# Kernel optimization log

Hardware: AMD Instinct MI355X
Metric: run time of the kernel (lower is better)

Reference implementation:

```python
import jax, jax.numpy as jnp
import numpy as np


def setup_inputs() -> dict:
    key = jax.random.key(0)
    ks = jax.random.split(key, 7)
    B, Hde, E, Hf, Wf, Catt = 256, 512, 512, 8, 32, 512
    return {
        "h": jax.random.normal(ks[0], (B, Hde), dtype=jnp.float32),
        "x_em": jax.random.normal(ks[1], (B, E, Hf, Wf), dtype=jnp.float32),
        "att_x_em": jax.random.normal(ks[2], (B, Hf * Wf, Catt), dtype=jnp.float32),
        "Wh": jax.random.normal(ks[3], (E, Hde), dtype=jnp.float32) * (1.0 / np.sqrt(Hde)),
        "bh": jax.random.normal(ks[4], (E,), dtype=jnp.float32) * 0.02,
        "Wa": jax.random.normal(ks[5], (E,), dtype=jnp.float32) * (1.0 / np.sqrt(E)),
        "ba": jax.random.normal(ks[6], (), dtype=jnp.float32) * 0.02,
        "feature_h": Hf,
        "feature_w": Wf,
    }


def reference(h, x_em, att_x_em, Wh, bh, Wa, ba, feature_h, feature_w):
    # h: [B, Hde]; 1x1 conv on [B,Hde,1,1] == linear layer
    B = h.shape[0]
    g_em = h @ Wh.T + bh                                   # [B, E]
    # broadcast-add g_em over spatial, tanh (dropout = identity in eval)
    feat = jnp.tanh(x_em + g_em[:, :, None, None])         # [B, E, H, W]
    # conv_att: 1x1 conv E -> 1 == weighted channel sum
    scores = jnp.einsum('behw,e->bhw', feat, Wa) + ba      # [B, H, W]
    alpha = jax.nn.softmax(scores.reshape(B, feature_h * feature_w), axis=-1)  # [B, HW]
    att_out = jnp.einsum('bs,bsc->bc', alpha, att_x_em)    # [B, Catt]
    return att_out, alpha.reshape(B, 1, feature_h * feature_w)
```

## Files before the change

kernel.cpp:

```cpp
#include <hip/hip_runtime.h>

#define BB 256
#define E 512
#define HDE 512
#define HW 256
#define CATT 512
#define EC 8
#define ECH (E / EC)
#define SC 8
#define SCH (HW / SC)


__device__ __forceinline__ float fast_tanh(float x) {
    float t = __expf(2.0f * x);
    return 1.0f - 2.0f / (t + 1.0f);
}

__global__ __launch_bounds__(256, 4) void kA(
        const float* __restrict__ h, const float* __restrict__ x_em,
        const float* __restrict__ Wh, const float* __restrict__ bh,
        const float* __restrict__ Wa, float* __restrict__ scoresPart) {
    const int b = blockIdx.x;
    const int ec = blockIdx.y;
    const int t = threadIdx.x;

    __shared__ float sH[HDE];
    __shared__ float sG[ECH];
    __shared__ float sWa[ECH];
    __shared__ float4 sPart[4][HW / 4];

    if (t < HDE / 4) {
        ((float4*)sH)[t] = ((const float4*)(h + (size_t)b * HDE))[t];
    }
    __syncthreads();

    {
        const int el = t >> 2;
        const int ks = t & 3;
        const int e = ec * ECH + el;
        const float* wrow = Wh + (size_t)e * HDE;
        float acc = 0.0f;
#pragma unroll
        for (int i = 0; i < HDE / 16; ++i) {
            const int k = ks * 4 + i * 16;
            float4 w = *(const float4*)(wrow + k);
            float4 hv = *(const float4*)(sH + k);
            acc += w.x * hv.x + w.y * hv.y + w.z * hv.z + w.w * hv.w;
        }
        acc += __shfl_xor(acc, 1);
        acc += __shfl_xor(acc, 2);
        if (ks == 0) {
            sG[el] = acc + bh[e];
            sWa[el] = Wa[e];
        }
    }
    __syncthreads();

    const int s4 = t & 63;
    const int esub = t >> 6;
    const float* xb = x_em + ((size_t)b * E + (size_t)ec * ECH) * HW + s4 * 4;
    float4 acc = {0.f, 0.f, 0.f, 0.f};
#pragma unroll 4
    for (int i = 0; i < ECH / 4; ++i) {
        const int el = 4 * i + esub;
        float4 x = *(const float4*)(xb + (size_t)el * HW);
        const float g = sG[el];
        const float wa = sWa[el];
        acc.x += wa * fast_tanh(x.x + g);
        acc.y += wa * fast_tanh(x.y + g);
        acc.z += wa * fast_tanh(x.z + g);
        acc.w += wa * fast_tanh(x.w + g);
    }

    sPart[esub][s4] = acc;
    __syncthreads();
    if (t < HW / 4) {
        float4 r0 = sPart[0][t], r1 = sPart[1][t], r2 = sPart[2][t], r3 = sPart[3][t];
        float4 r;
        r.x = r0.x + r1.x + r2.x + r3.x;
        r.y = r0.y + r1.y + r2.y + r3.y;
        r.z = r0.z + r1.z + r2.z + r3.z;
        r.w = r0.w + r1.w + r2.w + r3.w;
        *(float4*)(scoresPart + ((size_t)ec * BB + b) * HW + t * 4) = r;
    }
}

__global__ __launch_bounds__(256, 4) void kB(
        const float* __restrict__ scoresPart, float* __restrict__ out) {
    const int b = blockIdx.x;
    const int t = threadIdx.x;
    float v = 0.0f;
#pragma unroll
    for (int ec = 0; ec < EC; ++ec)
        v += scoresPart[((size_t)ec * BB + b) * HW + t];

    __shared__ float sred[4];
    const int wid = t >> 6;

    float m = v;
#pragma unroll
    for (int o = 32; o; o >>= 1) m = fmaxf(m, __shfl_xor(m, o));
    if ((t & 63) == 0) sred[wid] = m;
    __syncthreads();
    m = fmaxf(fmaxf(sred[0], sred[1]), fmaxf(sred[2], sred[3]));
    __syncthreads();

    float p = __expf(v - m);
    float s = p;
#pragma unroll
    for (int o = 32; o; o >>= 1) s += __shfl_xor(s, o);
    if ((t & 63) == 0) sred[wid] = s;
    __syncthreads();
    s = sred[0] + sred[1] + sred[2] + sred[3];

    out[(size_t)BB * CATT + (size_t)b * HW + t] = p / s;
}

__global__ __launch_bounds__(256, 8) void kC(
        const float* __restrict__ att, const float* __restrict__ alpha,
        float* __restrict__ outPart) {
    const int b = blockIdx.x;
    const int sc = blockIdx.y;
    const int t = threadIdx.x;
    const int c4 = t & 127;
    const int sp = t >> 7;

    __shared__ float sA[SCH];
    __shared__ float4 sP[CATT / 4];

    if (t < SCH) sA[t] = alpha[(size_t)b * HW + sc * SCH + t];
    __syncthreads();

    const float* ab = att + ((size_t)b * HW + (size_t)sc * SCH) * CATT + c4 * 4;
    float4 acc = {0.f, 0.f, 0.f, 0.f};
#pragma unroll 4
    for (int i = 0; i < SCH / 2; ++i) {
        const int s = 2 * i + sp;
        float4 x = *(const float4*)(ab + (size_t)s * CATT);
        const float a = sA[s];
        acc.x += a * x.x;
        acc.y += a * x.y;
        acc.z += a * x.z;
        acc.w += a * x.w;
    }
    if (sp == 1) sP[c4] = acc;
    __syncthreads();
    if (sp == 0) {
        float4 o = sP[c4];
        acc.x += o.x; acc.y += o.y; acc.z += o.z; acc.w += o.w;
        *(float4*)(outPart + ((size_t)sc * BB + b) * CATT + c4 * 4) = acc;
    }
}

__global__ __launch_bounds__(128, 8) void kD(
        const float* __restrict__ outPart, float* __restrict__ out) {
    const int b = blockIdx.x;
    const int t = threadIdx.x;
    float4 acc = {0.f, 0.f, 0.f, 0.f};
#pragma unroll
    for (int sc = 0; sc < SC; ++sc) {
        float4 x = *(const float4*)(outPart + ((size_t)sc * BB + b) * CATT + t * 4);
        acc.x += x.x; acc.y += x.y; acc.z += x.z; acc.w += x.w;
    }
    *(float4*)(out + (size_t)b * CATT + t * 4) = acc;
}

extern "C" void kernel_launch(void* const* d_in, const int* in_sizes, int n_in,
                              void* d_out, int out_size, void* d_ws, size_t ws_size,
                              hipStream_t stream) {
    const float* h      = (const float*)d_in[0];
    const float* x_em   = (const float*)d_in[1];
    const float* att    = (const float*)d_in[2];
    const float* Wh     = (const float*)d_in[3];
    const float* bh     = (const float*)d_in[4];
    const float* Wa     = (const float*)d_in[5];

    float* out = (float*)d_out;
    float* scoresPart = (float*)d_ws;
    float* outPart = (float*)d_ws + (size_t)EC * BB * HW;

    kA<<<dim3(BB, EC), 256, 0, stream>>>(h, x_em, Wh, bh, Wa, scoresPart);
    kB<<<dim3(BB), 256, 0, stream>>>(scoresPart, out);
    kC<<<dim3(BB, SC), 256, 0, stream>>>(att, out + (size_t)BB * CATT, outPart);
    kD<<<dim3(BB), 128, 0, stream>>>(outPart, out);
}
```

Measured before the change: 307.2 us.

## Fuse four attention kernels into one per-batch 1024-thread block

Replaces the four-kernel pipeline (score partials, softmax, weighted-sum partials, final reduction) with a single kernel. Each 1024-thread block handles one batch row end to end and keeps scores, alpha and partial sums in shared memory. This removes workspace round trips and three launch boundaries, and tanh now uses a hardware reciprocal. The cost is a grid of only 256 large blocks, with fewer waves in flight to hide memory latency and more per-block serialization between phases.

```diff
diff --git a/kernel.cpp b/kernel.cpp
--- a/kernel.cpp
+++ b/kernel.cpp
@@ -5,182 +5,142 @@
 #define HDE 512
 #define HW 256
 #define CATT 512
-#define EC 8
-#define ECH (E / EC)
-#define SC 8
-#define SCH (HW / SC)
-
+#define NT 1024
+#define NW (NT / 64)
 
 __device__ __forceinline__ float fast_tanh(float x) {
-    float t = __expf(2.0f * x);
-    return 1.0f - 2.0f / (t + 1.0f);
+    float e = __expf(2.0f * x);
+    float r = __builtin_amdgcn_rcpf(1.0f + e);
+    return 1.0f - 2.0f * r;
 }
 
-__global__ __launch_bounds__(256, 4) void kA(
+__global__ __launch_bounds__(NT, 4) void fused_attn(
         const float* __restrict__ h, const float* __restrict__ x_em,
-        const float* __restrict__ Wh, const float* __restrict__ bh,
-        const float* __restrict__ Wa, float* __restrict__ scoresPart) {
+        const float* __restrict__ att, const float* __restrict__ Wh,
+        const float* __restrict__ bh, const float* __restrict__ Wa,
+        float* __restrict__ out) {
     const int b = blockIdx.x;
-    const int ec = blockIdx.y;
     const int t = threadIdx.x;
+    const int lane = t & 63;
+    const int w = t >> 6;
 
     __shared__ float sH[HDE];
-    __shared__ float sG[ECH];
-    __shared__ float sWa[ECH];
-    __shared__ float4 sPart[4][HW / 4];
+    __shared__ float sG[E];
+    __shared__ float sWa[E];
+    __shared__ float sAlpha[HW];
+    __shared__ float sred[8];
+    __shared__ float4 sBuf4[NW * 64];
+    float* sBuf = (float*)sBuf4;
 
-    if (t < HDE / 4) {
+    if (t < HDE / 4)
         ((float4*)sH)[t] = ((const float4*)(h + (size_t)b * HDE))[t];
+    __syncthreads();
+
+    {
+        const int e = t >> 1;
+        const int half = t & 1;
+        const float* wrow = Wh + (size_t)e * HDE + half * (HDE / 2);
+        const float* hrow = sH + half * (HDE / 2);
+        float acc = 0.0f;
+#pragma unroll 8
+        for (int i = 0; i < HDE / 8; ++i) {
+            float4 wv = ((const float4*)wrow)[i];
+            float4 hv = ((const float4*)hrow)[i];
+            acc += wv.x * hv.x + wv.y * hv.y + wv.z * hv.z + wv.w * hv.w;
+        }
+        acc += __shfl_xor(acc, 1);
+        if (half == 0) {
+            sG[e] = acc + bh[e];
+            sWa[e] = Wa[e];
+        }
     }
     __syncthreads();
 
     {
-        const int el = t >> 2;
-        const int ks = t & 3;
-        const int e = ec * ECH + el;
-        const float* wrow = Wh + (size_t)e * HDE;
-        float acc = 0.0f;
-#pragma unroll
-        for (int i = 0; i < HDE / 16; ++i) {
-            const int k = ks * 4 + i * 16;
-            float4 w = *(const float4*)(wrow + k);
-            float4 hv = *(const float4*)(sH + k);
-            acc += w.x * hv.x + w.y * hv.y + w.z * hv.z + w.w * hv.w;
+        const float* xb = x_em + ((size_t)b * E + (size_t)w * (E / NW)) * HW + lane * 4;
+        float4 acc = {0.f, 0.f, 0.f, 0.f};
+#pragma unroll 8
+        for (int i = 0; i < E / NW; ++i) {
+            float4 x = *(const float4*)(xb + (size_t)i * HW);
+            const int e = w * (E / NW) + i;
+            const float g = sG[e];
+            const float wa = sWa[e];
+            acc.x += wa * fast_tanh(x.x + g);
+            acc.y += wa * fast_tanh(x.y + g);
+            acc.z += wa * fast_tanh(x.z + g);
+            acc.w += wa * fast_tanh(x.w + g);
         }
-        acc += __shfl_xor(acc, 1);
-        acc += __shfl_xor(acc, 2);
-        if (ks == 0) {
-            sG[el] = acc + bh[e];
-            sWa[el] = Wa[e];
-        }
+        sBuf4[w * 64 + lane] = acc;
     }
     __syncthreads();
 
-    const int s4 = t & 63;
-    const int esub = t >> 6;
-    const float* xb = x_em + ((size_t)b * E + (size_t)ec * ECH) * HW + s4 * 4;
-    float4 acc = {0.f, 0.f, 0.f, 0.f};
-#pragma unroll 4
-    for (int i = 0; i < ECH / 4; ++i) {
-        const int el = 4 * i + esub;
-        float4 x = *(const float4*)(xb + (size_t)el * HW);
-        const float g = sG[el];
-        const float wa = sWa[el];
-        acc.x += wa * fast_tanh(x.x + g);
-        acc.y += wa * fast_tanh(x.y + g);
-        acc.z += wa * fast_tanh(x.z + g);
-        acc.w += wa * fast_tanh(x.w + g);
+    float v = 0.f, p = 0.f;
+    if (t < HW) {
+        #pragma unroll
+        for (int g = 0; g < NW; ++g) v += sBuf[g * HW + t];
+        float m = v;
+        #pragma unroll
+        for (int o = 32; o; o >>= 1) m = fmaxf(m, __shfl_xor(m, o));
+        if (lane == 0) sred[w] = m;
     }
-
-    sPart[esub][s4] = acc;
     __syncthreads();
-    if (t < HW / 4) {
-        float4 r0 = sPart[0][t], r1 = sPart[1][t], r2 = sPart[2][t], r3 = sPart[3][t];
-        float4 r;
-        r.x = r0.x + r1.x + r2.x + r3.x;
-        r.y = r0.y + r1.y + r2.y + r3.y;
-        r.z = r0.z + r1.z + r2.z + r3.z;
-        r.w = r0.w + r1.w + r2.w + r3.w;
-        *(float4*)(scoresPart + ((size_t)ec * BB + b) * HW + t * 4) = r;
+    if (t < HW) {
+        float m = fmaxf(fmaxf(sred[0], sred[1]), fmaxf(sred[2], sred[3]));
+        p = __expf(v - m);
+        float s = p;
+        #pragma unroll
+        for (int o = 32; o; o >>= 1) s += __shfl_xor(s, o);
+        if (lane == 0) sred[4 + w] = s;
     }
-}
-
-__global__ __launch_bounds__(256, 4) void kB(
-        const float* __restrict__ scoresPart, float* __restrict__ out) {
-    const int b = blockIdx.x;
-    const int t = threadIdx.x;
-    float v = 0.0f;
-#pragma unroll
-    for (int ec = 0; ec < EC; ++ec)
-        v += scoresPart[((size_t)ec * BB + b) * HW + t];
-
-    __shared__ float sred[4];
-    const int wid = t >> 6;
-
-    float m = v;
-#pragma unroll
-    for (int o = 32; o; o >>= 1) m = fmaxf(m, __shfl_xor(m, o));
-    if ((t & 63) == 0) sred[wid] = m;
     __syncthreads();
-    m = fmaxf(fmaxf(sred[0], sred[1]), fmaxf(sred[2], sred[3]));
+    if (t < HW) {
+        float s = sred[4] + sred[5] + sred[6] + sred[7];
+        float a = p / s;
+        sAlpha[t] = a;
+        out[(size_t)BB * CATT + (size_t)b * HW + t] = a;
+    }
     __syncthreads();
 
-    float p = __expf(v - m);
-    float s = p;
-#pragma unroll
-    for (int o = 32; o; o >>= 1) s += __shfl_xor(s, o);
-    if ((t & 63) == 0) sred[wid] = s;
-    __syncthreads();
-    s = sred[0] + sred[1] + sred[2] + sred[3];
-
-    out[(size_t)BB * CATT + (size_t)b * HW + t] = p / s;
-}
-
-__global__ __launch_bounds__(256, 8) void kC(
-        const float* __restrict__ att, const float* __restrict__ alpha,
-        float* __restrict__ outPart) {
-    const int b = blockIdx.x;
-    const int sc = blockIdx.y;
-    const int t = threadIdx.x;
-    const int c4 = t & 127;
-    const int sp = t >> 7;
-
-    __shared__ float sA[SCH];
-    __shared__ float4 sP[CATT / 4];
-
-    if (t < SCH) sA[t] = alpha[(size_t)b * HW + sc * SCH + t];
+    {
+        const int c4 = t & 127;
+        const int g = t >> 7;
+        const float* ab = att + ((size_t)b * HW + g) * CATT + c4 * 4;
+        float4 acc = {0.f, 0.f, 0.f, 0.f};
+#pragma unroll 8
+        for (int i = 0; i < HW / 8; ++i) {
+            float4 x = *(const float4*)(ab + (size_t)i * 8 * CATT);
+            const float a = sAlpha[g + i * 8];
+            acc.x += a * x.x;
+            acc.y += a * x.y;
+            acc.z += a * x.z;
+            acc.w += a * x.w;
+        }
+        sBuf4[g * 128 + c4] = acc;
+    }
     __syncthreads();
 
-    const float* ab = att + ((size_t)b * HW + (size_t)sc * SCH) * CATT + c4 * 4;
-    float4 acc = {0.f, 0.f, 0.f, 0.f};
-#pragma unroll 4
-    for (int i = 0; i < SCH / 2; ++i) {
-        const int s = 2 * i + sp;
-        float4 x = *(const float4*)(ab + (size_t)s * CATT);
-        const float a = sA[s];
-        acc.x += a * x.x;
-        acc.y += a * x.y;
-        acc.z += a * x.z;
-        acc.w += a * x.w;
+    if (t < CATT / 4) {
+        float4 acc = sBuf4[t];
+        #pragma unroll
+        for (int g = 1; g < 8; ++g) {
+            float4 x = sBuf4[g * 128 + t];
+            acc.x += x.x; acc.y += x.y; acc.z += x.z; acc.w += x.w;
+        }
+        ((float4*)(out + (size_t)b * CATT))[t] = acc;
     }
-    if (sp == 1) sP[c4] = acc;
-    __syncthreads();
-    if (sp == 0) {
-        float4 o = sP[c4];
-        acc.x += o.x; acc.y += o.y; acc.z += o.z; acc.w += o.w;
-        *(float4*)(outPart + ((size_t)sc * BB + b) * CATT + c4 * 4) = acc;
-    }
-}
-
-__global__ __launch_bounds__(128, 8) void kD(
-        const float* __restrict__ outPart, float* __restrict__ out) {
-    const int b = blockIdx.x;
-    const int t = threadIdx.x;
-    float4 acc = {0.f, 0.f, 0.f, 0.f};
-#pragma unroll
-    for (int sc = 0; sc < SC; ++sc) {
-        float4 x = *(const float4*)(outPart + ((size_t)sc * BB + b) * CATT + t * 4);
-        acc.x += x.x; acc.y += x.y; acc.z += x.z; acc.w += x.w;
-    }
-    *(float4*)(out + (size_t)b * CATT + t * 4) = acc;
 }
 
 extern "C" void kernel_launch(void* const* d_in, const int* in_sizes, int n_in,
                               void* d_out, int out_size, void* d_ws, size_t ws_size,
                               hipStream_t stream) {
-    const float* h      = (const float*)d_in[0];
-    const float* x_em   = (const float*)d_in[1];
-    const float* att    = (const float*)d_in[2];
-    const float* Wh     = (const float*)d_in[3];
-    const float* bh     = (const float*)d_in[4];
-    const float* Wa     = (const float*)d_in[5];
+    const float* h    = (const float*)d_in[0];
+    const float* x_em = (const float*)d_in[1];
+    const float* att  = (const float*)d_in[2];
+    const float* Wh   = (const float*)d_in[3];
+    const float* bh   = (const float*)d_in[4];
+    const float* Wa   = (const float*)d_in[5];
 
     float* out = (float*)d_out;
-    float* scoresPart = (float*)d_ws;
-    float* outPart = (float*)d_ws + (size_t)EC * BB * HW;
 
-    kA<<<dim3(BB, EC), 256, 0, stream>>>(h, x_em, Wh, bh, Wa, scoresPart);
-    kB<<<dim3(BB), 256, 0, stream>>>(scoresPart, out);
-    kC<<<dim3(BB, SC), 256, 0, stream>>>(att, out + (size_t)BB * CATT, outPart);
-    kD<<<dim3(BB), 128, 0, stream>>>(outPart, out);
+    fused_attn<<<dim3(BB), NT, 0, stream>>>(h, x_em, att, Wh, bh, Wa, out);
 }
```

After: 318.6 us. +3.7%, slower.
